# Performance work log

Measured on AMD Instinct MI355X. Metric: run time of the kernel, lower is better.

The kernel has to match this reference:

```python
import jax, jax.numpy as jnp
import numpy as np

NUM_HEADS = 16
HEAD_DIM = 80
HIDDEN = 1280
SEQ = 3072
NUM_SEGS = 6  # 6 packed images of 512 patches each


def rotate_half(x):
    x1, x2 = jnp.split(x, 2, axis=-1)
    return jnp.concatenate([-x2, x1], axis=-1)


def setup_inputs() -> dict:
    key = jax.random.key(0)
    ks = jax.random.split(key, 6)
    hidden_states = jax.random.normal(ks[0], (SEQ, HIDDEN), dtype=jnp.float32)
    # RoPE tables as in Qwen-VL vision: freqs over half the head_dim, duplicated
    half = HEAD_DIM // 2
    inv_freq = 1.0 / (10000.0 ** (jnp.arange(half, dtype=jnp.float32) / half))
    pos = jnp.arange(SEQ, dtype=jnp.float32)[:, None]
    freqs = pos * inv_freq[None, :]                      # (SEQ, half)
    emb = jnp.concatenate([freqs, freqs], axis=-1)       # (SEQ, HEAD_DIM)
    cos = jnp.cos(emb)
    sin = jnp.sin(emb)
    # Packed segment boundaries: [0, 512, 1024, ..., 3072]
    cu_seqlens = jnp.arange(0, SEQ + 1, SEQ // NUM_SEGS, dtype=jnp.int32)
    scale = 0.02
    w_qkv = jax.random.normal(ks[1], (3 * HIDDEN, HIDDEN), dtype=jnp.float32) * scale
    b_qkv = jax.random.normal(ks[2], (3 * HIDDEN,), dtype=jnp.float32) * scale
    w_proj = jax.random.normal(ks[3], (HIDDEN, HIDDEN), dtype=jnp.float32) * scale
    b_proj = jax.random.normal(ks[4], (HIDDEN,), dtype=jnp.float32) * scale
    return {
        "hidden_states": hidden_states, "cos": cos, "sin": sin,
        "w_qkv": w_qkv, "b_qkv": b_qkv, "w_proj": w_proj, "b_proj": b_proj,
        "cu_seqlens": cu_seqlens,
    }


def reference(hidden_states, cos, sin, w_qkv, b_qkv, w_proj, b_proj, cu_seqlens):
    S, H = hidden_states.shape
    nh, hd = NUM_HEADS, H // NUM_HEADS

    # Fused QKV projection: (S, 3H) -> q, k, v each (S, nh, hd)
    qkv = hidden_states @ w_qkv.T + b_qkv
    qkv = qkv.reshape(S, 3, nh, hd)
    q, k, v = qkv[:, 0], qkv[:, 1], qkv[:, 2]

    # Inline RoPE on q/k (cos/sin broadcast over heads)
    c = cos[:, None, :]
    s = sin[:, None, :]
    q = q * c + rotate_half(q) * s
    k = k * c + rotate_half(k) * s

    # Original casts fp32 -> fp16 for the flash attention kernel
    q16 = q.astype(jnp.float16)
    k16 = k.astype(jnp.float16)
    v16 = v.astype(jnp.float16)

    # Varlen masking: tokens attend only within their own packed segment
    tok = jnp.arange(S)
    seg = jnp.searchsorted(cu_seqlens, tok, side="right")  # (S,)
    same_seg = seg[:, None] == seg[None, :]                 # (S, S)

    scale = hd ** (-0.5)
    # Scores accumulated in fp32 (as flash attention does internally)
    scores = jnp.einsum("qhd,khd->hqk", q16, k16,
                        preferred_element_type=jnp.float32) * scale
    scores = jnp.where(same_seg[None], scores, jnp.finfo(jnp.float32).min)
    weights = jax.nn.softmax(scores, axis=-1).astype(jnp.float16)  # (nh, S, S)

    attn = jnp.einsum("hqk,khd->qhd", weights, v16)  # (S, nh, hd) fp16
    attn = attn.astype(jnp.float32).reshape(S, H)
    return attn @ w_proj.T + b_proj
```

## Files before the change

kernel.cpp:

```cpp
#include <hip/hip_runtime.h>

typedef _Float16 f16;
typedef _Float16 half8 __attribute__((ext_vector_type(8)));
typedef _Float16 half4 __attribute__((ext_vector_type(4)));
typedef float f32x4 __attribute__((ext_vector_type(4)));

__device__ __forceinline__ void gld_lds16(const void* g, void* l) {
  __builtin_amdgcn_global_load_lds((const __attribute__((address_space(1))) void*)g,
                                   (__attribute__((address_space(3))) void*)l, 16, 0, 0);
}

template <int CTRL>
__device__ __forceinline__ float dppf(float x) {
  return __builtin_bit_cast(float,
      __builtin_amdgcn_mov_dpp(__builtin_bit_cast(int, x), CTRL, 0xf, 0xf, true));
}
__device__ __forceinline__ float dpp_max16(float v) {
  v = fmaxf(v, dppf<0xB1>(v));
  v = fmaxf(v, dppf<0x4E>(v));
  v = fmaxf(v, dppf<0x128>(v));
  v = fmaxf(v, dppf<0x140>(v));
  return v;
}
__device__ __forceinline__ float dpp_sum16(float v) {
  v += dppf<0xB1>(v);
  v += dppf<0x4E>(v);
  v += dppf<0x128>(v);
  v += dppf<0x140>(v);
  return v;
}

__global__ void cvt_all(const float* __restrict__ hid, const float* __restrict__ wq,
                        const float* __restrict__ wp, f16* __restrict__ hid16,
                        f16* __restrict__ wq16, f16* __restrict__ wp16) {
  int b = blockIdx.x;
  const float* in;
  f16* out;
  int i;
  if (b < 3840) { in = hid; out = hid16; i = b * 256 + threadIdx.x; }
  else if (b < 8640) { in = wq; out = wq16; i = (b - 3840) * 256 + threadIdx.x; }
  else { in = wp; out = wp16; i = (b - 8640) * 256 + threadIdx.x; }
  float4 v = ((const float4*)in)[i];
  half4 o;
  o.x = (f16)v.x; o.y = (f16)v.y; o.z = (f16)v.z; o.w = (f16)v.w;
  ((half4*)out)[i] = o;
}

template <bool OUT_F16>
__global__ __launch_bounds__(256, 2) void gemm_bt(const f16* __restrict__ A,
                                                  const f16* __restrict__ B,
                                                  const float* __restrict__ bias,
                                                  void* __restrict__ Cout,
                                                  int K, int lda, int ldb, int ldc) {
  __shared__ f16 As[128 * 32];
  __shared__ f16 Bs[128 * 32];
  const int tid = threadIdx.x, lane = tid & 63, wave = tid >> 6;
  const int bm = blockIdx.x * 128, bn = blockIdx.y * 128;
  const int wm = (wave & 1) * 64, wn = (wave >> 1) * 64;
  const int lm = lane & 15, kq = (lane >> 4) * 8;
  const int arow = tid >> 2, acol = (tid & 3) * 8;

  const f16* Ab = A + (size_t)(bm + arow) * lda + acol;
  const f16* Bb = B + (size_t)(bn + arow) * ldb + acol;
  f16* AsW = As + wave * 512;
  f16* BsW = Bs + wave * 512;

  f32x4 acc[4][4] = {};
  for (int k0 = 0; k0 < K; k0 += 32) {
    gld_lds16(Ab + k0, AsW);
    gld_lds16(Ab + (size_t)64 * lda + k0, AsW + 2048);
    gld_lds16(Bb + k0, BsW);
    gld_lds16(Bb + (size_t)64 * ldb + k0, BsW + 2048);
    __syncthreads();
    half8 af[4], bf[4];
#pragma unroll
    for (int mt = 0; mt < 4; mt++) af[mt] = *(const half8*)&As[(wm + 16 * mt + lm) * 32 + kq];
#pragma unroll
    for (int nt = 0; nt < 4; nt++) bf[nt] = *(const half8*)&Bs[(wn + 16 * nt + lm) * 32 + kq];
#pragma unroll
    for (int mt = 0; mt < 4; mt++)
#pragma unroll
      for (int nt = 0; nt < 4; nt++)
        acc[mt][nt] = __builtin_amdgcn_mfma_f32_16x16x32_f16(af[mt], bf[nt], acc[mt][nt], 0, 0, 0);
    __syncthreads();
  }
  const int q4 = lane >> 4;
#pragma unroll
  for (int mt = 0; mt < 4; mt++)
#pragma unroll
    for (int nt = 0; nt < 4; nt++)
#pragma unroll
      for (int r = 0; r < 4; r++) {
        int gr = bm + wm + 16 * mt + 4 * q4 + r;
        int gc = bn + wn + 16 * nt + lm;
        float v = acc[mt][nt][r] + bias[gc];
        if (OUT_F16)
          ((f16*)Cout)[(size_t)gr * ldc + gc] = (f16)v;
        else
          ((float*)Cout)[(size_t)gr * ldc + gc] = v;
      }
}

template <bool OUT_F16>
__global__ __launch_bounds__(256, 2) void gemm_bt64(const f16* __restrict__ A,
                                                    const f16* __restrict__ B,
                                                    const float* __restrict__ bias,
                                                    void* __restrict__ Cout,
                                                    int K, int lda, int ldb, int ldc) {
  __shared__ f16 As[64 * 32];
  __shared__ f16 Bs[128 * 32];
  const int tid = threadIdx.x, lane = tid & 63, wave = tid >> 6;
  const int bm = blockIdx.x * 64, bn = blockIdx.y * 128;
  const int wm = (wave & 1) * 32, wn = (wave >> 1) * 64;
  const int lm = lane & 15, kq = (lane >> 4) * 8;
  const int arow = tid >> 2, acol = (tid & 3) * 8;

  const f16* Ab = A + (size_t)(bm + arow) * lda + acol;
  const f16* Bb = B + (size_t)(bn + arow) * ldb + acol;
  f16* AsW = As + wave * 512;
  f16* BsW = Bs + wave * 512;

  f32x4 acc[2][4] = {};
  for (int k0 = 0; k0 < K; k0 += 32) {
    gld_lds16(Ab + k0, AsW);
    gld_lds16(Bb + k0, BsW);
    gld_lds16(Bb + (size_t)64 * ldb + k0, BsW + 2048);
    __syncthreads();
    half8 af[2], bf[4];
#pragma unroll
    for (int mt = 0; mt < 2; mt++) af[mt] = *(const half8*)&As[(wm + 16 * mt + lm) * 32 + kq];
#pragma unroll
    for (int nt = 0; nt < 4; nt++) bf[nt] = *(const half8*)&Bs[(wn + 16 * nt + lm) * 32 + kq];
#pragma unroll
    for (int mt = 0; mt < 2; mt++)
#pragma unroll
      for (int nt = 0; nt < 4; nt++)
        acc[mt][nt] = __builtin_amdgcn_mfma_f32_16x16x32_f16(af[mt], bf[nt], acc[mt][nt], 0, 0, 0);
    __syncthreads();
  }
  const int q4 = lane >> 4;
#pragma unroll
  for (int mt = 0; mt < 2; mt++)
#pragma unroll
    for (int nt = 0; nt < 4; nt++)
#pragma unroll
      for (int r = 0; r < 4; r++) {
        int gr = bm + wm + 16 * mt + 4 * q4 + r;
        int gc = bn + wn + 16 * nt + lm;
        float v = acc[mt][nt][r] + bias[gc];
        if (OUT_F16)
          ((f16*)Cout)[(size_t)gr * ldc + gc] = (f16)v;
        else
          ((float*)Cout)[(size_t)gr * ldc + gc] = v;
      }
}

__global__ void rope_transpose(f16* __restrict__ qkv, const float* __restrict__ cosb,
                               const float* __restrict__ sinb, f16* __restrict__ vt) {
  __shared__ f16 tile[64][72];
  const int b = blockIdx.x;
  if (b < 1920) {
    int idx = b * 256 + threadIdx.x;
    int c = idx % 5;
    int t = idx / 5;
    int h = t % 16; t /= 16;
    int qk = t & 1;
    int s = t >> 1;
    size_t base = (size_t)s * 3840 + qk * 1280 + h * 80 + c * 8;
    half8 x = *(half8*)&qkv[base];
    half8 y = *(half8*)&qkv[base + 40];
    const float* cp = cosb + s * 80 + c * 8;
    const float* sp = sinb + s * 80 + c * 8;
    half8 ox, oy;
#pragma unroll
    for (int i = 0; i < 8; i++) {
      float cs = cp[i], sn = sp[i];
      float xf = (float)x[i], yf = (float)y[i];
      ox[i] = (f16)(xf * cs - yf * sn);
      oy[i] = (f16)(yf * cs + xf * sn);
    }
    *(half8*)&qkv[base] = ox;
    *(half8*)&qkv[base + 40] = oy;
  } else {
    const int bb = b - 1920;
    const int bs = (bb % 48) * 64;
    const int bd = (bb / 48) * 64;
    const int r = threadIdx.x >> 2, c = (threadIdx.x & 3) * 16;
    *(uint4*)&tile[r][c] = *(const uint4*)&qkv[(size_t)(bs + r) * 3840 + 2560 + bd + c];
    *(uint4*)&tile[r][c + 8] = *(const uint4*)&qkv[(size_t)(bs + r) * 3840 + 2560 + bd + c + 8];
    __syncthreads();
    f16 tmp[16];
#pragma unroll
    for (int i = 0; i < 16; i++) tmp[i] = tile[c + i][r];
    *(uint4*)&vt[(size_t)(bd + r) * 3072 + bs + c] = *(uint4*)&tmp[0];
    *(uint4*)&vt[(size_t)(bd + r) * 3072 + bs + c + 8] = *(uint4*)&tmp[8];
  }
}

__global__ __launch_bounds__(256, 3) void flash_attn4(const f16* __restrict__ qkv,
                                                      const f16* __restrict__ vt,
                                                      f16* __restrict__ attn) {
  constexpr int KS = 84;
  constexpr int VS = 132;
  __shared__ f16 KP[128 * KS + 96];
  __shared__ f16 Vb[80 * VS + 16];
  const int tid = threadIdx.x, lane = tid & 63, wave = tid >> 6;
  const int lm = lane & 15, q4 = lane >> 4;
  const int h = blockIdx.x, g = blockIdx.z;
  const int qbase = g * 512 + blockIdx.y * 64 + wave * 16;
  f16* P = KP + wave * (16 * VS);
  const half8 hz = {};

  const f16* qrow = qkv + (size_t)(qbase + lm) * 3840 + h * 80;
  half8 qf[3];
  qf[0] = *(const half8*)(qrow + q4 * 8);
  qf[1] = *(const half8*)(qrow + 32 + q4 * 8);
  qf[2] = (q4 < 2) ? *(const half8*)(qrow + 64 + q4 * 8) : hz;

  int ko[5], kl[5], vo[5], vl[5];
#pragma unroll
  for (int i = 0; i < 5; i++) {
    int task = tid + 256 * i;
    int krr = task / 10, kcc = task % 10;
    ko[i] = krr * 3840 + kcc * 8;
    kl[i] = krr * KS + kcc * 8;
    int vrr = task >> 4, vcc = task & 15;
    vo[i] = vrr * 3072 + vcc * 8;
    vl[i] = vrr * VS + vcc * 8;
  }
  const f16* kseg = qkv + (size_t)g * 512 * 3840 + 1280 + h * 80;
  const f16* vseg = vt + (size_t)h * 80 * 3072 + g * 512;

  uint4 kpf[5], vpf[5];
#pragma unroll
  for (int i = 0; i < 5; i++) kpf[i] = *(const uint4*)(kseg + ko[i]);
#pragma unroll
  for (int i = 0; i < 5; i++) vpf[i] = *(const uint4*)(vseg + vo[i]);

  f32x4 oacc[5] = {};
  float mprev[4] = {-1e30f, -1e30f, -1e30f, -1e30f};
  float lsum[4] = {0.f, 0.f, 0.f, 0.f};
  const float sc = 0.11180339887498949f * 1.4426950408889634f;

  for (int j = 0; j < 4; j++) {
    __syncthreads();
#pragma unroll
    for (int i = 0; i < 5; i++) *(uint4*)&KP[kl[i]] = kpf[i];
#pragma unroll
    for (int i = 0; i < 5; i++) *(uint4*)&Vb[vl[i]] = vpf[i];
    __syncthreads();

    f32x4 sacc[8] = {};
#pragma unroll
    for (int ks = 0; ks < 3; ks++) {
      half8 bk[8];
#pragma unroll
      for (int nt = 0; nt < 8; nt++)
        bk[nt] = (ks < 2 || q4 < 2)
                     ? *(const half8*)&KP[(16 * nt + lm) * KS + 32 * ks + q4 * 8]
                     : hz;
#pragma unroll
      for (int nt = 0; nt < 8; nt++)
        sacc[nt] = __builtin_amdgcn_mfma_f32_16x16x32_f16(qf[ks], bk[nt], sacc[nt], 0, 0, 0);
    }

    float mnew[4], alpha[4], rs[4];
#pragma unroll
    for (int r = 0; r < 4; r++) {
      float v = fmaxf(fmaxf(fmaxf(sacc[0][r], sacc[1][r]), fmaxf(sacc[2][r], sacc[3][r])),
                      fmaxf(fmaxf(sacc[4][r], sacc[5][r]), fmaxf(sacc[6][r], sacc[7][r])));
      v = dpp_max16(v);
      mnew[r] = fmaxf(mprev[r], v * sc);
      alpha[r] = __builtin_exp2f(mprev[r] - mnew[r]);
      mprev[r] = mnew[r];
      rs[r] = 0.f;
    }
#pragma unroll
    for (int nt = 0; nt < 8; nt++)
#pragma unroll
      for (int r = 0; r < 4; r++) {
        float p = __builtin_exp2f(sacc[nt][r] * sc - mnew[r]);
        sacc[nt][r] = p;
        rs[r] += p;
      }
#pragma unroll
    for (int r = 0; r < 4; r++) {
      float v = dpp_sum16(rs[r]);
      lsum[r] = alpha[r] * lsum[r] + v;
#pragma unroll
      for (int nt2 = 0; nt2 < 5; nt2++) oacc[nt2][r] *= alpha[r];
    }

    __syncthreads();
#pragma unroll
    for (int nt = 0; nt < 8; nt++)
#pragma unroll
      for (int r = 0; r < 4; r++)
        P[(4 * q4 + r) * VS + 16 * nt + lm] = (f16)sacc[nt][r];

    if (j < 3) {
      const f16* kn = kseg + (size_t)(j + 1) * (128 * 3840);
      const f16* vn = vseg + (j + 1) * 128;
#pragma unroll
      for (int i = 0; i < 5; i++) kpf[i] = *(const uint4*)(kn + ko[i]);
#pragma unroll
      for (int i = 0; i < 5; i++) vpf[i] = *(const uint4*)(vn + vo[i]);
    }

#pragma unroll
    for (int ks = 0; ks < 4; ks++) {
      half8 ap = *(const half8*)&P[lm * VS + ks * 32 + q4 * 8];
      half8 bv[5];
#pragma unroll
      for (int nt2 = 0; nt2 < 5; nt2++)
        bv[nt2] = *(const half8*)&Vb[(16 * nt2 + lm) * VS + ks * 32 + q4 * 8];
#pragma unroll
      for (int nt2 = 0; nt2 < 5; nt2++)
        oacc[nt2] = __builtin_amdgcn_mfma_f32_16x16x32_f16(ap, bv[nt2], oacc[nt2], 0, 0, 0);
    }
  }
#pragma unroll
  for (int r = 0; r < 4; r++) {
    float inv = 1.0f / lsum[r];
    int s = qbase + 4 * q4 + r;
#pragma unroll
    for (int nt2 = 0; nt2 < 5; nt2++)
      attn[(size_t)s * 1280 + h * 80 + 16 * nt2 + lm] = (f16)(oacc[nt2][r] * inv);
  }
}

extern "C" void kernel_launch(void* const* d_in, const int* in_sizes, int n_in,
                              void* d_out, int out_size, void* d_ws, size_t ws_size,
                              hipStream_t stream) {
  const float* hidden = (const float*)d_in[0];
  const float* cosb   = (const float*)d_in[1];
  const float* sinb   = (const float*)d_in[2];
  const float* w_qkv  = (const float*)d_in[3];
  const float* b_qkv  = (const float*)d_in[4];
  const float* w_proj = (const float*)d_in[5];
  const float* b_proj = (const float*)d_in[6];

  char* ws = (char*)d_ws;
  f16* hidden16 = (f16*)(ws + 0);
  f16* wqkv16   = (f16*)(ws + 7864320);
  f16* wproj16  = (f16*)(ws + 17694720);
  f16* qkv16    = (f16*)(ws + 20971520);
  f16* attn16   = (f16*)(ws + 44564480);
  f16* vt16     = hidden16;

  cvt_all<<<10240, 256, 0, stream>>>(hidden, w_qkv, w_proj, hidden16, wqkv16, wproj16);

  gemm_bt<true><<<dim3(24, 30), 256, 0, stream>>>(hidden16, wqkv16, b_qkv, qkv16,
                                                  1280, 1280, 1280, 3840);

  rope_transpose<<<2880, 256, 0, stream>>>(qkv16, cosb, sinb, vt16);

  flash_attn4<<<dim3(16, 8, 6), 256, 0, stream>>>(qkv16, vt16, attn16);

  gemm_bt64<false><<<dim3(48, 10), 256, 0, stream>>>(attn16, wproj16, b_proj, d_out,
                                                     1280, 1280, 1280, 1280);
}
```

Measured before the change: 228.3 us.

## Load attention K/V tiles directly into LDS via global_load_lds and raise occupancy

The attention kernel now loads K and V tiles straight from global memory into LDS with the global_load_lds builtin, replacing register prefetch followed by LDS stores. The LDS layout becomes unpadded, with K at row stride 80 and V at row stride 128, and the P buffer aliases the K region. Launch bounds rise from 3 to 4 blocks per SM. The goal is fewer VGPRs and fewer LDS store instructions, giving higher occupancy. In exchange, the next tile is no longer prefetched during the PV compute, and the unpadded strides may cause LDS bank conflicts.

```diff
diff --git a/kernel.cpp b/kernel.cpp
--- a/kernel.cpp
+++ b/kernel.cpp
@@ -197,18 +197,17 @@
   }
 }
 
-__global__ __launch_bounds__(256, 3) void flash_attn4(const f16* __restrict__ qkv,
+__global__ __launch_bounds__(256, 4) void flash_attn5(const f16* __restrict__ qkv,
                                                       const f16* __restrict__ vt,
                                                       f16* __restrict__ attn) {
-  constexpr int KS = 84;
-  constexpr int VS = 132;
-  __shared__ f16 KP[128 * KS + 96];
-  __shared__ f16 Vb[80 * VS + 16];
+  __shared__ f16 S[20480];
+  f16* Ks = S;
+  f16* Vs = S + 10240;
   const int tid = threadIdx.x, lane = tid & 63, wave = tid >> 6;
   const int lm = lane & 15, q4 = lane >> 4;
   const int h = blockIdx.x, g = blockIdx.z;
   const int qbase = g * 512 + blockIdx.y * 64 + wave * 16;
-  f16* P = KP + wave * (16 * VS);
+  f16* P = S + wave * 2112;
   const half8 hz = {};
 
   const f16* qrow = qkv + (size_t)(qbase + lm) * 3840 + h * 80;
@@ -217,25 +216,15 @@
   qf[1] = *(const half8*)(qrow + 32 + q4 * 8);
   qf[2] = (q4 < 2) ? *(const half8*)(qrow + 64 + q4 * 8) : hz;
 
-  int ko[5], kl[5], vo[5], vl[5];
+  size_t kgo[5], vgo[5];
 #pragma unroll
   for (int i = 0; i < 5; i++) {
-    int task = tid + 256 * i;
-    int krr = task / 10, kcc = task % 10;
-    ko[i] = krr * 3840 + kcc * 8;
-    kl[i] = krr * KS + kcc * 8;
-    int vrr = task >> 4, vcc = task & 15;
-    vo[i] = vrr * 3072 + vcc * 8;
-    vl[i] = vrr * VS + vcc * 8;
-  }
-  const f16* kseg = qkv + (size_t)g * 512 * 3840 + 1280 + h * 80;
-  const f16* vseg = vt + (size_t)h * 80 * 3072 + g * 512;
-
-  uint4 kpf[5], vpf[5];
-#pragma unroll
-  for (int i = 0; i < 5; i++) kpf[i] = *(const uint4*)(kseg + ko[i]);
-#pragma unroll
-  for (int i = 0; i < 5; i++) vpf[i] = *(const uint4*)(vseg + vo[i]);
+    int t = (wave * 5 + i) * 1024 + lane * 16;
+    int kr = t / 160, kcb = t % 160;
+    kgo[i] = (size_t)(g * 512 + kr) * 3840 + 1280 + h * 80 + (kcb >> 1);
+    int vd = t >> 8, vsb = t & 255;
+    vgo[i] = (size_t)(h * 80 + vd) * 3072 + g * 512 + (vsb >> 1);
+  }
 
   f32x4 oacc[5] = {};
   float mprev[4] = {-1e30f, -1e30f, -1e30f, -1e30f};
@@ -245,9 +234,11 @@
   for (int j = 0; j < 4; j++) {
     __syncthreads();
 #pragma unroll
-    for (int i = 0; i < 5; i++) *(uint4*)&KP[kl[i]] = kpf[i];
-#pragma unroll
-    for (int i = 0; i < 5; i++) *(uint4*)&Vb[vl[i]] = vpf[i];
+    for (int i = 0; i < 5; i++) {
+      int chunk = wave * 5 + i;
+      gld_lds16(qkv + kgo[i] + (size_t)j * (128 * 3840), Ks + chunk * 512);
+      gld_lds16(vt + vgo[i] + j * 128, Vs + chunk * 512);
+    }
     __syncthreads();
 
     f32x4 sacc[8] = {};
@@ -257,7 +248,7 @@
 #pragma unroll
       for (int nt = 0; nt < 8; nt++)
         bk[nt] = (ks < 2 || q4 < 2)
-                     ? *(const half8*)&KP[(16 * nt + lm) * KS + 32 * ks + q4 * 8]
+                     ? *(const half8*)&Ks[(16 * nt + lm) * 80 + 32 * ks + q4 * 8]
                      : hz;
 #pragma unroll
       for (int nt = 0; nt < 8; nt++)
@@ -296,24 +287,15 @@
     for (int nt = 0; nt < 8; nt++)
 #pragma unroll
       for (int r = 0; r < 4; r++)
-        P[(4 * q4 + r) * VS + 16 * nt + lm] = (f16)sacc[nt][r];
-
-    if (j < 3) {
-      const f16* kn = kseg + (size_t)(j + 1) * (128 * 3840);
-      const f16* vn = vseg + (j + 1) * 128;
-#pragma unroll
-      for (int i = 0; i < 5; i++) kpf[i] = *(const uint4*)(kn + ko[i]);
-#pragma unroll
-      for (int i = 0; i < 5; i++) vpf[i] = *(const uint4*)(vn + vo[i]);
-    }
+        P[(4 * q4 + r) * 132 + 16 * nt + lm] = (f16)sacc[nt][r];
 
 #pragma unroll
     for (int ks = 0; ks < 4; ks++) {
-      half8 ap = *(const half8*)&P[lm * VS + ks * 32 + q4 * 8];
+      half8 ap = *(const half8*)&P[lm * 132 + ks * 32 + q4 * 8];
       half8 bv[5];
 #pragma unroll
       for (int nt2 = 0; nt2 < 5; nt2++)
-        bv[nt2] = *(const half8*)&Vb[(16 * nt2 + lm) * VS + ks * 32 + q4 * 8];
+        bv[nt2] = *(const half8*)&Vs[(16 * nt2 + lm) * 128 + ks * 32 + q4 * 8];
 #pragma unroll
       for (int nt2 = 0; nt2 < 5; nt2++)
         oacc[nt2] = __builtin_amdgcn_mfma_f32_16x16x32_f16(ap, bv[nt2], oacc[nt2], 0, 0, 0);
@@ -355,7 +337,7 @@
 
   rope_transpose<<<2880, 256, 0, stream>>>(qkv16, cosb, sinb, vt16);
 
-  flash_attn4<<<dim3(16, 8, 6), 256, 0, stream>>>(qkv16, vt16, attn16);
+  flash_attn5<<<dim3(16, 8, 6), 256, 0, stream>>>(qkv16, vt16, attn16);
 
   gemm_bt64<false><<<dim3(48, 10), 256, 0, stream>>>(attn16, wproj16, b_proj, d_out,
                                                      1280, 1280, 1280, 1280);
```

Measured after the change: 211.0 us. 7.6% less time.
